# Optimization experiments

Measured on AMD Instinct MI355X. Metric: run time of the kernel, lower is better.

## Reference

```python
import jax, jax.numpy as jnp
import numpy as np


def _forward(x, wc, we, Wb1, bb1, Wb2, bb2, Wr1, br1, Wr2, br2,
             Wq1, bq1, Wq2, bq2, Wq3, bq3, Wo1, bo1, Wo2, bo2, Wo3, bo3, scale):
    bs, c, h, w = x.shape
    Hs, Ws = scale * h, scale * w
    fh = (jnp.arange(Hs, dtype=jnp.float32) + 0.5) / scale
    fw = (jnp.arange(Ws, dtype=jnp.float32) + 0.5) / scale
    coor_h = fh - jnp.floor(fh + 0.001) - 0.5  # [Hs] fractional phase
    coor_w = fw - jnp.floor(fw + 0.001) - 0.5  # [Ws]
    ones_hw = jnp.ones((Hs, Ws), jnp.float32)
    meta = jnp.stack([ones_hw, ones_hw / scale,
                      jnp.broadcast_to(coor_h[:, None], (Hs, Ws)),
                      jnp.broadcast_to(coor_w[None, :], (Hs, Ws))], 0)  # [4,Hs,Ws]
    chan_mean = x.mean(axis=(0, 2, 3))  # [c]
    chan_scale = jnp.concatenate([chan_mean[:, None], jnp.ones((c, 3), jnp.float32)], axis=1)  # [c,4]
    inp = meta[None] * chan_scale[:, :, None, None]  # [c,4,Hs,Ws]

    # body: 1x1x1 Conv3d over spectral-channel axis c
    lin = lambda W, b, t: jnp.einsum('oc,cfhw->ofhw', W, t) + b[:, None, None, None]
    emb = jax.nn.relu(lin(Wb2, bb2, jax.nn.relu(lin(Wb1, bb1, inp))))  # [c,4,Hs,Ws]

    # offset head: Conv2d 1x1 with batch = c, features = 4 -> 2
    lin2 = lambda W, b, t: jnp.einsum('of,cfhw->cohw', W, t) + b[None, :, None, None]
    off = lin2(Wo3, bo3, jax.nn.relu(lin2(Wo2, bo2, jax.nn.relu(lin2(Wo1, bo1, emb)))))  # [c,2,Hs,Ws]

    # routing_1: Conv3d over c -> 1 channel, sigmoid
    r = jax.nn.sigmoid(lin(Wr2, br2, jax.nn.relu(lin(Wr1, br1, emb))))[0]  # [4,Hs,Ws]
    # routing_2: Conv2d 1x1 over the 4 meta-features -> E experts
    lin3 = lambda W, b, t: jnp.einsum('of,fhw->ohw', W, t) + b[:, None, None]
    rw = jax.nn.sigmoid(lin3(Wq3, bq3, jax.nn.relu(lin3(Wq2, bq2, jax.nn.relu(lin3(Wq1, bq1, r))))))  # [E,Hs,Ws]

    # per-channel offset grid_sample (bilinear, zeros padding, align_corners=True)
    px0 = fw - 0.5  # [Ws] base source x coord
    py0 = fh - 0.5  # [Hs]

    def sample(img, offx, offy):  # img [bs,h,w]; off* [Hs,Ws]
        px = px0[None, :] + offx
        py = py0[:, None] + offy
        x0 = jnp.floor(px); y0 = jnp.floor(py)
        wx = px - x0; wy = py - y0
        x0i = x0.astype(jnp.int32); y0i = y0.astype(jnp.int32)
        def g(yi, xi):
            v = ((xi >= 0) & (xi <= w - 1) & (yi >= 0) & (yi <= h - 1)).astype(img.dtype)
            return img[:, jnp.clip(yi, 0, h - 1), jnp.clip(xi, 0, w - 1)] * v[None]
        return (g(y0i, x0i) * ((1 - wy) * (1 - wx))[None]
                + g(y0i, x0i + 1) * ((1 - wy) * wx)[None]
                + g(y0i + 1, x0i) * (wy * (1 - wx))[None]
                + g(y0i + 1, x0i + 1) * (wy * wx)[None])

    fea0 = jax.vmap(lambda xi, oi: sample(xi, oi[0], oi[1]),
                    in_axes=(1, 0), out_axes=1)(x, off)  # [bs,c,Hs,Ws]

    # per-pixel expert-mixed compress/expand: (sum_e r_e Wc_e) f then (sum_e r_e We_e)
    mid = jnp.einsum('ehw,ekc,bchw->bkhw', rw, wc, fea0)   # [bs,c//8,Hs,Ws]
    out = jnp.einsum('ehw,eck,bkhw->bchw', rw, we, mid)    # [bs,c,Hs,Ws]
    return out + fea0


def setup_inputs() -> dict:
    key = jax.random.key(0)
    ks = jax.random.split(key, 32)
    bs, c, h, w = 4, 64, 64, 64
    E, k = 4, c // 8
    s = 0.05
    d = {
        'x': jax.random.normal(ks[0], (bs, c, h, w), jnp.float32),
        'wc': jax.random.normal(ks[1], (E, k, c), jnp.float32) * s,
        'we': jax.random.normal(ks[2], (E, c, k), jnp.float32) * s,
        'Wb1': jax.random.normal(ks[3], (c, c), jnp.float32) * s,
        'bb1': jax.random.normal(ks[4], (c,), jnp.float32) * s,
        'Wb2': jax.random.normal(ks[5], (c, c), jnp.float32) * s,
        'bb2': jax.random.normal(ks[6], (c,), jnp.float32) * s,
        'Wr1': jax.random.normal(ks[7], (64, c), jnp.float32) * s,
        'br1': jax.random.normal(ks[8], (64,), jnp.float32) * s,
        'Wr2': jax.random.normal(ks[9], (1, 64), jnp.float32) * s,
        'br2': jax.random.normal(ks[10], (1,), jnp.float32) * s,
        'Wq1': jax.random.normal(ks[11], (64, 4), jnp.float32) * s,
        'bq1': jax.random.normal(ks[12], (64,), jnp.float32) * s,
        'Wq2': jax.random.normal(ks[13], (64, 64), jnp.float32) * s,
        'bq2': jax.random.normal(ks[14], (64,), jnp.float32) * s,
        'Wq3': jax.random.normal(ks[15], (E, 64), jnp.float32) * s,
        'bq3': jax.random.normal(ks[16], (E,), jnp.float32) * s,
        'Wo1': jax.random.normal(ks[17], (64, 4), jnp.float32) * s,
        'bo1': jax.random.normal(ks[18], (64,), jnp.float32) * s,
        'Wo2': jax.random.normal(ks[19], (64, 64), jnp.float32) * s,
        'bo2': jax.random.normal(ks[20], (64,), jnp.float32) * s,
        'Wo3': jax.random.normal(ks[21], (2, 64), jnp.float32) * s,
        'bo3': jax.random.normal(ks[22], (2,), jnp.float32) * s,
        'scale': 4,
    }
    return d


def reference(x, wc, we, Wb1, bb1, Wb2, bb2, Wr1, br1, Wr2, br2,
              Wq1, bq1, Wq2, bq2, Wq3, bq3, Wo1, bo1, Wo2, bo2, Wo3, bo3, scale):
    return _forward(x, wc, we, Wb1, bb1, Wb2, bb2, Wr1, br1, Wr2, br2,
                    Wq1, bq1, Wq2, bq2, Wq3, bq3, Wo1, bo1, Wo2, bo2, Wo3, bo3, int(scale))
```

## Files before the change

### kernel.cpp

```cpp
#include <hip/hip_runtime.h>


__device__ __forceinline__ float relu_(float v){ return fmaxf(v, 0.f); }
__device__ __forceinline__ float sigm_(float v){ return 1.f/(1.f + __expf(-v)); }

__global__ void k_mean(const float* __restrict__ x, float* __restrict__ ws) {
  const int ch = blockIdx.x, t = threadIdx.x;
  float s = 0.f;
  for (int b = 0; b < 4; ++b) {
    const float4* p = reinterpret_cast<const float4*>(x + (size_t)(b*64 + ch)*4096);
    for (int idx = t; idx < 1024; idx += 256) { float4 v = p[idx]; s += (v.x+v.y)+(v.z+v.w); }
  }
  __shared__ float red[256];
  red[t] = s; __syncthreads();
  for (int off = 128; off > 0; off >>= 1) {
    if (t < off) red[t] += red[t + off];
    __syncthreads();
  }
  if (t == 0) ws[ch] = red[0] * (1.f/16384.f);
}

__launch_bounds__(256)
__global__ void k_phase(const float* __restrict__ wc, const float* __restrict__ we,
    const float* __restrict__ Wb1, const float* __restrict__ bb1,
    const float* __restrict__ Wb2, const float* __restrict__ bb2,
    const float* __restrict__ Wr1, const float* __restrict__ br1,
    const float* __restrict__ Wr2, const float* __restrict__ br2,
    const float* __restrict__ Wq1, const float* __restrict__ bq1,
    const float* __restrict__ Wq2, const float* __restrict__ bq2,
    const float* __restrict__ Wq3, const float* __restrict__ bq3,
    const float* __restrict__ Wo1, const float* __restrict__ bo1,
    const float* __restrict__ Wo2, const float* __restrict__ bo2,
    const float* __restrict__ Wo3, const float* __restrict__ bo3,
    float* __restrict__ ws)
{
  const int p = blockIdx.x, pi = p >> 2, pj = p & 3;
  const int t = threadIdx.x;
  const float chv = 0.25f*pi - 0.375f, cwv = 0.25f*pj - 0.375f;

  __shared__ __align__(16) float WbT1[4096];
  __shared__ __align__(16) float WbT2[4096];
  __shared__ __align__(16) float WrT1[4096];
  __shared__ __align__(16) float WqT2[4096];
  __shared__ __align__(16) float Wo2L[4096];
  __shared__ __align__(16) float Wo1L[256];
  __shared__ float Wo3L[128];
  __shared__ float bo1L[64], bo2L[64];

  __shared__ float meanL[64];
  __shared__ __align__(16) float t1L[64][4];
  __shared__ __align__(16) float embL[64][4];
  __shared__ __align__(16) float rpL[64][4];
  __shared__ float r4[4];
  __shared__ float q1L[64], q2L[64];
  __shared__ float rwL[4];
  __shared__ float oxL[64][4], oyL[64][4];

  {
    const float* srcs[4] = {Wb1, Wb2, Wr1, Wq2};
    float* dsts[4] = {WbT1, WbT2, WrT1, WqT2};
    for (int m = 0; m < 4; ++m) {
      const float4* W4 = reinterpret_cast<const float4*>(srcs[m]);
      float* WT = dsts[m];
      for (int v = t; v < 1024; v += 256) {
        float4 d = W4[v];
        int r = v >> 4, c = (v & 15) << 2;
        WT[(c+0)*64 + r] = d.x;
        WT[(c+1)*64 + r] = d.y;
        WT[(c+2)*64 + r] = d.z;
        WT[(c+3)*64 + r] = d.w;
      }
    }
    for (int v = t; v < 1024; v += 256)
      reinterpret_cast<float4*>(Wo2L)[v] = reinterpret_cast<const float4*>(Wo2)[v];
    if (t < 64) {
      reinterpret_cast<float4*>(Wo1L)[t] = reinterpret_cast<const float4*>(Wo1)[t];
      bo1L[t] = bo1[t]; bo2L[t] = bo2[t];
      meanL[t] = ws[t];
    }
    if (t >= 64 && t < 192) Wo3L[t-64] = Wo3[t-64];
  }
  __syncthreads();

  if (t < 64) {
    float a0 = 0.f, as = 0.f;
    #pragma unroll 8
    for (int c = 0; c < 64; ++c) { float w = WbT1[c*64+t]; a0 += w*meanL[c]; as += w; }
    float bb = bb1[t];
    t1L[t][0] = relu_(a0 + bb);
    t1L[t][1] = relu_(0.25f*as + bb);
    t1L[t][2] = relu_(chv*as + bb);
    t1L[t][3] = relu_(cwv*as + bb);
  }
  __syncthreads();
  if (t < 64) {
    float bb = bb2[t];
    float e0=bb,e1=bb,e2=bb,e3=bb;
    #pragma unroll 8
    for (int c = 0; c < 64; ++c) {
      float w = WbT2[c*64+t];
      float4 tv = *reinterpret_cast<const float4*>(&t1L[c][0]);
      e0 += w*tv.x; e1 += w*tv.y; e2 += w*tv.z; e3 += w*tv.w;
    }
    embL[t][0]=relu_(e0); embL[t][1]=relu_(e1); embL[t][2]=relu_(e2); embL[t][3]=relu_(e3);
  }
  __syncthreads();
  if (t < 64) {
    float bb = br1[t];
    float p0=bb,p1=bb,p2=bb,p3=bb;
    #pragma unroll 8
    for (int c = 0; c < 64; ++c) {
      float w = WrT1[c*64+t];
      float4 ev = *reinterpret_cast<const float4*>(&embL[c][0]);
      p0 += w*ev.x; p1 += w*ev.y; p2 += w*ev.z; p3 += w*ev.w;
    }
    rpL[t][0]=relu_(p0); rpL[t][1]=relu_(p1); rpL[t][2]=relu_(p2); rpL[t][3]=relu_(p3);
  }
  __syncthreads();
  if (t < 4) {
    float acc = br2[0];
    #pragma unroll
    for (int c = 0; c < 64; ++c) acc += Wr2[c]*rpL[c][t];
    r4[t] = sigm_(acc);
  }
  __syncthreads();
  if (t < 64) {
    float acc = bq1[t];
    #pragma unroll
    for (int f = 0; f < 4; ++f) acc += Wq1[t*4+f]*r4[f];
    q1L[t] = relu_(acc);
  }
  __syncthreads();
  if (t < 64) {
    float acc = bq2[t];
    #pragma unroll 8
    for (int c = 0; c < 64; ++c) acc += WqT2[c*64+t]*q1L[c];
    q2L[t] = relu_(acc);
  }
  __syncthreads();
  if (t < 4) {
    float acc = bq3[t];
    #pragma unroll
    for (int c = 0; c < 64; ++c) acc += Wq3[t*64+c]*q2L[c];
    rwL[t] = sigm_(acc);
  }
  __syncthreads();

  {
    const int ch = t & 63, q = t >> 6;
    const float4 e = *reinterpret_cast<const float4*>(&embL[ch][0]);
    float v1[64];
    #pragma unroll
    for (int o = 0; o < 64; ++o) {
      float4 w = *reinterpret_cast<const float4*>(&Wo1L[o*4]);
      v1[o] = relu_(w.x*e.x + w.y*e.y + w.z*e.z + w.w*e.w + bo1L[o]);
    }
    float ox = 0.f, oy = 0.f;
    for (int o = q*16; o < q*16+16; ++o) {
      float acc = bo2L[o];
      const float4* row = reinterpret_cast<const float4*>(&Wo2L[o*64]);
      #pragma unroll
      for (int k = 0; k < 16; ++k) {
        float4 w = row[k];
        acc += w.x*v1[4*k+0] + w.y*v1[4*k+1] + w.z*v1[4*k+2] + w.w*v1[4*k+3];
      }
      acc = relu_(acc);
      ox += Wo3L[o]*acc;
      oy += Wo3L[64+o]*acc;
    }
    oxL[ch][q] = ox; oyL[ch][q] = oy;
  }
  __syncthreads();

  float* ws_off = ws + 64;
  float* ws_wcT = ws + 2112;
  float* ws_weT = ws + 10304;
  if (t < 64) {
    ws_off[(p*64+t)*2+0] = oxL[t][0]+oxL[t][1]+oxL[t][2]+oxL[t][3] + bo3[0];
    ws_off[(p*64+t)*2+1] = oyL[t][0]+oyL[t][1]+oyL[t][2]+oyL[t][3] + bo3[1];
  }
  const float r0 = rwL[0], r1 = rwL[1], r2 = rwL[2], r3 = rwL[3];
  for (int idx = t; idx < 512; idx += 256) {
    const int ch = idx >> 3, k = idx & 7;
    ws_wcT[p*512 + idx] = r0*wc[(0*8+k)*64+ch] + r1*wc[(1*8+k)*64+ch]
                        + r2*wc[(2*8+k)*64+ch] + r3*wc[(3*8+k)*64+ch];
    ws_weT[p*512 + idx] = r0*we[(0*64+ch)*8+k] + r1*we[(1*64+ch)*8+k]
                        + r2*we[(2*64+ch)*8+k] + r3*we[(3*64+ch)*8+k];
  }
}

__launch_bounds__(256, 4)
__global__ void k_main(const float* __restrict__ x, const float* __restrict__ ws,
                       float* __restrict__ out) {
  const int i = blockIdx.x;
  const int b = blockIdx.y;
  const int j = threadIdx.x;
  const int pi = i & 3;
  const int pj = j & 3;

  __shared__ float wcT[4*520];
  __shared__ float weT[4*520];
  __shared__ float offxL[4*68];
  __shared__ int4  rowi[256];

  const float* wsoff = ws + 64;
  const float* wswc  = ws + 2112;
  const float* wswe  = ws + 10304;

  for (int idx = threadIdx.x; idx < 2048; idx += 256) {
    const int ph = idx >> 9, rem = idx & 511;
    wcT[ph*520 + rem] = wswc[(pi*4 + ph)*512 + rem];
    weT[ph*520 + rem] = wswe[(pi*4 + ph)*512 + rem];
  }
  {
    const int ch = threadIdx.x >> 2, ph = threadIdx.x & 3;
    const int p = pi*4 + ph;
    const float ox = wsoff[(p*64 + ch)*2 + 0];
    const float oy = wsoff[(p*64 + ch)*2 + 1];
    offxL[ph*68 + ch] = ox;
    const float py = i*0.25f - 0.375f + oy;
    const float fy = floorf(py);
    const float wy = py - fy;
    const int y0 = (int)fy, y1 = y0 + 1;
    const int y0c = min(max(y0, 0), 63), y1c = min(max(y1, 0), 63);
    const float wy0 = ((unsigned)y0 <= 63u) ? (1.f - wy) : 0.f;
    const float wy1 = ((unsigned)y1 <= 63u) ? wy : 0.f;
    rowi[ch*4 + ph] = make_int4(ch*4096 + y0c*64, ch*4096 + y1c*64,
                                __float_as_int(wy0), __float_as_int(wy1));
  }
  __syncthreads();

  const float* __restrict__ xb = x + (size_t)b*64*4096;
  const float px0 = j*0.25f - 0.375f;

  float fea[64];
  float mid[8] = {0.f,0.f,0.f,0.f,0.f,0.f,0.f,0.f};

  #pragma unroll
  for (int ch = 0; ch < 64; ++ch) {
    const int4 ri = rowi[ch*4 + pj];
    const float px = px0 + offxL[pj*68 + ch];
    const float fx = floorf(px);
    const float wx = px - fx;
    const int x0 = (int)fx, x1 = x0 + 1;
    const int x0c = min(max(x0, 0), 63), x1c = min(max(x1, 0), 63);
    const float wx0 = ((unsigned)x0 <= 63u) ? (1.f - wx) : 0.f;
    const float wx1 = ((unsigned)x1 <= 63u) ? wx : 0.f;
    const float g00 = xb[ri.x + x0c], g01 = xb[ri.x + x1c];
    const float g10 = xb[ri.y + x0c], g11 = xb[ri.y + x1c];
    const float f0 = g00*wx0 + g01*wx1;
    const float f1 = g10*wx0 + g11*wx1;
    const float fv = f0*__int_as_float(ri.z) + f1*__int_as_float(ri.w);
    fea[ch] = fv;
    const float4* wcv = reinterpret_cast<const float4*>(&wcT[pj*520 + ch*8]);
    const float4 wa = wcv[0], wb = wcv[1];
    mid[0] += wa.x*fv; mid[1] += wa.y*fv; mid[2] += wa.z*fv; mid[3] += wa.w*fv;
    mid[4] += wb.x*fv; mid[5] += wb.y*fv; mid[6] += wb.z*fv; mid[7] += wb.w*fv;
  }

  const int obase = (b*64)*65536 + i*256 + j;
  #pragma unroll
  for (int ch = 0; ch < 64; ++ch) {
    const float4* wev = reinterpret_cast<const float4*>(&weT[pj*520 + ch*8]);
    const float4 wa = wev[0], wb = wev[1];
    float acc = fea[ch];
    acc += wa.x*mid[0] + wa.y*mid[1] + wa.z*mid[2] + wa.w*mid[3];
    acc += wb.x*mid[4] + wb.y*mid[5] + wb.z*mid[6] + wb.w*mid[7];
    out[obase + ch*65536] = acc;
  }
}

extern "C" void kernel_launch(void* const* d_in, const int* in_sizes, int n_in,
                              void* d_out, int out_size, void* d_ws, size_t ws_size,
                              hipStream_t stream) {
  const float* x   = (const float*)d_in[0];
  const float* wc  = (const float*)d_in[1];
  const float* we  = (const float*)d_in[2];
  const float* Wb1 = (const float*)d_in[3];
  const float* bb1 = (const float*)d_in[4];
  const float* Wb2 = (const float*)d_in[5];
  const float* bb2 = (const float*)d_in[6];
  const float* Wr1 = (const float*)d_in[7];
  const float* br1 = (const float*)d_in[8];
  const float* Wr2 = (const float*)d_in[9];
  const float* br2 = (const float*)d_in[10];
  const float* Wq1 = (const float*)d_in[11];
  const float* bq1 = (const float*)d_in[12];
  const float* Wq2 = (const float*)d_in[13];
  const float* bq2 = (const float*)d_in[14];
  const float* Wq3 = (const float*)d_in[15];
  const float* bq3 = (const float*)d_in[16];
  const float* Wo1 = (const float*)d_in[17];
  const float* bo1 = (const float*)d_in[18];
  const float* Wo2 = (const float*)d_in[19];
  const float* bo2 = (const float*)d_in[20];
  const float* Wo3 = (const float*)d_in[21];
  const float* bo3 = (const float*)d_in[22];
  float* ws  = (float*)d_ws;
  float* out = (float*)d_out;

  k_mean<<<64, 256, 0, stream>>>(x, ws);
  k_phase<<<16, 256, 0, stream>>>(wc, we, Wb1, bb1, Wb2, bb2, Wr1, br1, Wr2, br2,
                                  Wq1, bq1, Wq2, bq2, Wq3, bq3,
                                  Wo1, bo1, Wo2, bo2, Wo3, bo3, ws);
  k_main<<<dim3(256, 4), 256, 0, stream>>>(x, ws, out);
}
```

Measured before the change: 164.3 us.

## Split channel-mean over batch, stage phase weights in padded LDS, tweak main bounds

The channel-mean kernel now launches one block per (channel, batch) and writes partial sums, which the phase kernel combines, giving more parallelism to the reduction. The phase kernel stores weight matrices row-major with padding 66 instead of transposed, and caches biases, wc/we and the small routing weights in LDS rather than reading them from global memory. The main kernel's launch bounds drop from 4 to 3 blocks per SM to allow more registers, and its pointer arithmetic is hoisted. Each change targets a different part of the pipeline, and lowering the occupancy hint could reduce latency hiding in the memory-bound main kernel.

```diff
diff --git a/kernel.cpp b/kernel.cpp
--- a/kernel.cpp
+++ b/kernel.cpp
@@ -5,19 +5,18 @@
 __device__ __forceinline__ float sigm_(float v){ return 1.f/(1.f + __expf(-v)); }
 
 __global__ void k_mean(const float* __restrict__ x, float* __restrict__ ws) {
-  const int ch = blockIdx.x, t = threadIdx.x;
-  float s = 0.f;
-  for (int b = 0; b < 4; ++b) {
-    const float4* p = reinterpret_cast<const float4*>(x + (size_t)(b*64 + ch)*4096);
-    for (int idx = t; idx < 1024; idx += 256) { float4 v = p[idx]; s += (v.x+v.y)+(v.z+v.w); }
-  }
+  const int ch = blockIdx.x, b = blockIdx.y, t = threadIdx.x;
+  const float4* p = reinterpret_cast<const float4*>(x + (size_t)(b*64 + ch)*4096);
+  float4 v0 = p[t], v1 = p[t+256], v2 = p[t+512], v3 = p[t+768];
+  float s = ((v0.x+v0.y)+(v0.z+v0.w)) + ((v1.x+v1.y)+(v1.z+v1.w))
+          + ((v2.x+v2.y)+(v2.z+v2.w)) + ((v3.x+v3.y)+(v3.z+v3.w));
   __shared__ float red[256];
   red[t] = s; __syncthreads();
   for (int off = 128; off > 0; off >>= 1) {
     if (t < off) red[t] += red[t + off];
     __syncthreads();
   }
-  if (t == 0) ws[ch] = red[0] * (1.f/16384.f);
+  if (t == 0) ws[18496 + b*64 + ch] = red[0];
 }
 
 __launch_bounds__(256)
@@ -38,13 +37,18 @@
   const int t = threadIdx.x;
   const float chv = 0.25f*pi - 0.375f, cwv = 0.25f*pj - 0.375f;
 
-  __shared__ __align__(16) float WbT1[4096];
-  __shared__ __align__(16) float WbT2[4096];
-  __shared__ __align__(16) float WrT1[4096];
-  __shared__ __align__(16) float WqT2[4096];
+  __shared__ float WbL1[64*66];
+  __shared__ float WbL2[64*66];
+  __shared__ float WrL1[64*66];
+  __shared__ float WqL2[64*66];
   __shared__ __align__(16) float Wo2L[4096];
   __shared__ __align__(16) float Wo1L[256];
+  __shared__ __align__(16) float wcL[2048];
+  __shared__ __align__(16) float weL[2048];
   __shared__ float Wo3L[128];
+  __shared__ float Wq1L[256], Wq3L[256];
+  __shared__ float Wr2L[64];
+  __shared__ float bb1L[64], bb2L[64], br1L[64], bq1L[64], bq2L[64];
   __shared__ float bo1L[64], bo2L[64];
 
   __shared__ float meanL[64];
@@ -58,25 +62,33 @@
 
   {
     const float* srcs[4] = {Wb1, Wb2, Wr1, Wq2};
-    float* dsts[4] = {WbT1, WbT2, WrT1, WqT2};
+    float* dsts[4] = {WbL1, WbL2, WrL1, WqL2};
     for (int m = 0; m < 4; ++m) {
       const float4* W4 = reinterpret_cast<const float4*>(srcs[m]);
-      float* WT = dsts[m];
+      float* WL = dsts[m];
       for (int v = t; v < 1024; v += 256) {
         float4 d = W4[v];
-        int r = v >> 4, c = (v & 15) << 2;
-        WT[(c+0)*64 + r] = d.x;
-        WT[(c+1)*64 + r] = d.y;
-        WT[(c+2)*64 + r] = d.z;
-        WT[(c+3)*64 + r] = d.w;
+        const int r = v >> 4, c = (v & 15) << 2;
+        float* q = &WL[r*66 + c];
+        q[0] = d.x; q[1] = d.y; q[2] = d.z; q[3] = d.w;
       }
     }
     for (int v = t; v < 1024; v += 256)
       reinterpret_cast<float4*>(Wo2L)[v] = reinterpret_cast<const float4*>(Wo2)[v];
+    for (int v = t; v < 512; v += 256) {
+      reinterpret_cast<float4*>(wcL)[v] = reinterpret_cast<const float4*>(wc)[v];
+      reinterpret_cast<float4*>(weL)[v] = reinterpret_cast<const float4*>(we)[v];
+    }
     if (t < 64) {
       reinterpret_cast<float4*>(Wo1L)[t] = reinterpret_cast<const float4*>(Wo1)[t];
+      reinterpret_cast<float4*>(Wq1L)[t] = reinterpret_cast<const float4*>(Wq1)[t];
+      reinterpret_cast<float4*>(Wq3L)[t] = reinterpret_cast<const float4*>(Wq3)[t];
+      bb1L[t] = bb1[t]; bb2L[t] = bb2[t]; br1L[t] = br1[t];
+      bq1L[t] = bq1[t]; bq2L[t] = bq2[t];
       bo1L[t] = bo1[t]; bo2L[t] = bo2[t];
-      meanL[t] = ws[t];
+      Wr2L[t] = Wr2[t];
+      const float* wsp = ws + 18496;
+      meanL[t] = (wsp[t] + wsp[64+t] + wsp[128+t] + wsp[192+t]) * (1.f/16384.f);
     }
     if (t >= 64 && t < 192) Wo3L[t-64] = Wo3[t-64];
   }
@@ -84,9 +96,10 @@
 
   if (t < 64) {
     float a0 = 0.f, as = 0.f;
-    #pragma unroll 8
-    for (int c = 0; c < 64; ++c) { float w = WbT1[c*64+t]; a0 += w*meanL[c]; as += w; }
-    float bb = bb1[t];
+    const float* row = &WbL1[t*66];
+    #pragma unroll 8
+    for (int c = 0; c < 64; ++c) { float w = row[c]; a0 += w*meanL[c]; as += w; }
+    float bb = bb1L[t];
     t1L[t][0] = relu_(a0 + bb);
     t1L[t][1] = relu_(0.25f*as + bb);
     t1L[t][2] = relu_(chv*as + bb);
@@ -94,11 +107,12 @@
   }
   __syncthreads();
   if (t < 64) {
-    float bb = bb2[t];
+    float bb = bb2L[t];
     float e0=bb,e1=bb,e2=bb,e3=bb;
+    const float* row = &WbL2[t*66];
     #pragma unroll 8
     for (int c = 0; c < 64; ++c) {
-      float w = WbT2[c*64+t];
+      float w = row[c];
       float4 tv = *reinterpret_cast<const float4*>(&t1L[c][0]);
       e0 += w*tv.x; e1 += w*tv.y; e2 += w*tv.z; e3 += w*tv.w;
     }
@@ -106,11 +120,12 @@
   }
   __syncthreads();
   if (t < 64) {
-    float bb = br1[t];
+    float bb = br1L[t];
     float p0=bb,p1=bb,p2=bb,p3=bb;
+    const float* row = &WrL1[t*66];
     #pragma unroll 8
     for (int c = 0; c < 64; ++c) {
-      float w = WrT1[c*64+t];
+      float w = row[c];
       float4 ev = *reinterpret_cast<const float4*>(&embL[c][0]);
       p0 += w*ev.x; p1 += w*ev.y; p2 += w*ev.z; p3 += w*ev.w;
     }
@@ -119,29 +134,30 @@
   __syncthreads();
   if (t < 4) {
     float acc = br2[0];
+    #pragma unroll 8
+    for (int c = 0; c < 64; ++c) acc += Wr2L[c]*rpL[c][t];
+    r4[t] = sigm_(acc);
+  }
+  __syncthreads();
+  if (t < 64) {
+    float acc = bq1L[t];
     #pragma unroll
-    for (int c = 0; c < 64; ++c) acc += Wr2[c]*rpL[c][t];
-    r4[t] = sigm_(acc);
-  }
-  __syncthreads();
-  if (t < 64) {
-    float acc = bq1[t];
-    #pragma unroll
-    for (int f = 0; f < 4; ++f) acc += Wq1[t*4+f]*r4[f];
+    for (int f = 0; f < 4; ++f) acc += Wq1L[t*4+f]*r4[f];
     q1L[t] = relu_(acc);
   }
   __syncthreads();
   if (t < 64) {
-    float acc = bq2[t];
-    #pragma unroll 8
-    for (int c = 0; c < 64; ++c) acc += WqT2[c*64+t]*q1L[c];
+    float acc = bq2L[t];
+    const float* row = &WqL2[t*66];
+    #pragma unroll 8
+    for (int c = 0; c < 64; ++c) acc += row[c]*q1L[c];
     q2L[t] = relu_(acc);
   }
   __syncthreads();
   if (t < 4) {
     float acc = bq3[t];
-    #pragma unroll
-    for (int c = 0; c < 64; ++c) acc += Wq3[t*64+c]*q2L[c];
+    #pragma unroll 8
+    for (int c = 0; c < 64; ++c) acc += Wq3L[t*64+c]*q2L[c];
     rwL[t] = sigm_(acc);
   }
   __syncthreads();
@@ -182,14 +198,14 @@
   const float r0 = rwL[0], r1 = rwL[1], r2 = rwL[2], r3 = rwL[3];
   for (int idx = t; idx < 512; idx += 256) {
     const int ch = idx >> 3, k = idx & 7;
-    ws_wcT[p*512 + idx] = r0*wc[(0*8+k)*64+ch] + r1*wc[(1*8+k)*64+ch]
-                        + r2*wc[(2*8+k)*64+ch] + r3*wc[(3*8+k)*64+ch];
-    ws_weT[p*512 + idx] = r0*we[(0*64+ch)*8+k] + r1*we[(1*64+ch)*8+k]
-                        + r2*we[(2*64+ch)*8+k] + r3*we[(3*64+ch)*8+k];
+    ws_wcT[p*512 + idx] = r0*wcL[(0*8+k)*64+ch] + r1*wcL[(1*8+k)*64+ch]
+                        + r2*wcL[(2*8+k)*64+ch] + r3*wcL[(3*8+k)*64+ch];
+    ws_weT[p*512 + idx] = r0*weL[(0*64+ch)*8+k] + r1*weL[(1*64+ch)*8+k]
+                        + r2*weL[(2*64+ch)*8+k] + r3*weL[(3*64+ch)*8+k];
   }
 }
 
-__launch_bounds__(256, 4)
+__launch_bounds__(256, 3)
 __global__ void k_main(const float* __restrict__ x, const float* __restrict__ ws,
                        float* __restrict__ out) {
   const int i = blockIdx.x;
@@ -236,10 +252,14 @@
   float fea[64];
   float mid[8] = {0.f,0.f,0.f,0.f,0.f,0.f,0.f,0.f};
 
+  const float4* wc_pj = reinterpret_cast<const float4*>(&wcT[pj*520]);
+  const float* offx_pj = &offxL[pj*68];
+  const int4* rowi_pj = &rowi[pj];
+
   #pragma unroll
   for (int ch = 0; ch < 64; ++ch) {
-    const int4 ri = rowi[ch*4 + pj];
-    const float px = px0 + offxL[pj*68 + ch];
+    const int4 ri = rowi_pj[ch*4];
+    const float px = px0 + offx_pj[ch];
     const float fx = floorf(px);
     const float wx = px - fx;
     const int x0 = (int)fx, x1 = x0 + 1;
@@ -252,21 +272,20 @@
     const float f1 = g10*wx0 + g11*wx1;
     const float fv = f0*__int_as_float(ri.z) + f1*__int_as_float(ri.w);
     fea[ch] = fv;
-    const float4* wcv = reinterpret_cast<const float4*>(&wcT[pj*520 + ch*8]);
-    const float4 wa = wcv[0], wb = wcv[1];
+    const float4 wa = wc_pj[ch*2], wb = wc_pj[ch*2+1];
     mid[0] += wa.x*fv; mid[1] += wa.y*fv; mid[2] += wa.z*fv; mid[3] += wa.w*fv;
     mid[4] += wb.x*fv; mid[5] += wb.y*fv; mid[6] += wb.z*fv; mid[7] += wb.w*fv;
   }
 
-  const int obase = (b*64)*65536 + i*256 + j;
+  const float4* we_pj = reinterpret_cast<const float4*>(&weT[pj*520]);
+  float* op = out + (size_t)(b*64)*65536 + i*256 + j;
   #pragma unroll
   for (int ch = 0; ch < 64; ++ch) {
-    const float4* wev = reinterpret_cast<const float4*>(&weT[pj*520 + ch*8]);
-    const float4 wa = wev[0], wb = wev[1];
+    const float4 wa = we_pj[ch*2], wb = we_pj[ch*2+1];
     float acc = fea[ch];
     acc += wa.x*mid[0] + wa.y*mid[1] + wa.z*mid[2] + wa.w*mid[3];
     acc += wb.x*mid[4] + wb.y*mid[5] + wb.z*mid[6] + wb.w*mid[7];
-    out[obase + ch*65536] = acc;
+    op[ch*65536] = acc;
   }
 }
 
@@ -299,7 +318,7 @@
   float* ws  = (float*)d_ws;
   float* out = (float*)d_out;
 
-  k_mean<<<64, 256, 0, stream>>>(x, ws);
+  k_mean<<<dim3(64, 4), 256, 0, stream>>>(x, ws);
   k_phase<<<16, 256, 0, stream>>>(wc, we, Wb1, bb1, Wb2, bb2, Wr1, br1, Wr2, br2,
                                   Wq1, bq1, Wq2, bq2, Wq3, bq3,
                                   Wo1, bo1, Wo2, bo2, Wo3, bo3, ws);
```

Result: faster. 160.8 us (-2.1%).
